# Kernel tuning notes

Hardware: AMD Instinct MI355X
Metric: run time of the kernel (lower is better)

The kernel has to match this reference:

```python
import jax, jax.numpy as jnp
import numpy as np

NUM_HEADS = 8
HEAD_DIM = 64  # joiner_dim 512 / 8
LN_EPS = 1e-5


def _layer_norm(x, g, b):
    mu = jnp.mean(x, axis=-1, keepdims=True)
    var = jnp.mean(jnp.square(x - mu), axis=-1, keepdims=True)
    return (x - mu) * jax.lax.rsqrt(var + LN_EPS) * g + b


def setup_inputs() -> dict:
    key = jax.random.key(0)
    ks = jax.random.split(key, 24)
    N, T, S = 16, 512, 5
    E, D, J, V = 512, 512, 512, 2000
    s = 0.02
    inp = {
        "encoder_out": jax.random.normal(ks[0], (N, T, S, E), jnp.float32),
        "decoder_out": jax.random.normal(ks[1], (N, T, S, D), jnp.float32),
        # ScaledLinear projections (initial_scale absorbed into weights)
        "We": jax.random.normal(ks[2], (J, E), jnp.float32) * s * 0.25,
        "be": jnp.zeros((J,), jnp.float32),
        "Wd": jax.random.normal(ks[3], (J, D), jnp.float32) * s * 0.25,
        "bd": jnp.zeros((J,), jnp.float32),
        # LayerNorms
        "g_q": jnp.ones((J,), jnp.float32),
        "beta_q": jnp.zeros((J,), jnp.float32),
        "g_kv": jnp.ones((J,), jnp.float32),
        "beta_kv": jnp.zeros((J,), jnp.float32),
        # attention projections (xavier-ish)
        "Wq": jax.random.normal(ks[4], (J, J), jnp.float32) * s,
        "bq": jnp.zeros((J,), jnp.float32),
        "Wk": jax.random.normal(ks[5], (J, J), jnp.float32) * s,
        "bk": jnp.zeros((J,), jnp.float32),
        "Wv": jax.random.normal(ks[6], (J, J), jnp.float32) * s,
        "bv": jnp.zeros((J,), jnp.float32),
        "Wo": jax.random.normal(ks[7], (J, J), jnp.float32) * s,
        "bo": jnp.zeros((J,), jnp.float32),
        # final vocab projection
        "Wout": jax.random.normal(ks[8], (V, J), jnp.float32) * s,
        "bout": jnp.zeros((V,), jnp.float32),
    }
    return inp


def reference(encoder_out, decoder_out, We, be, Wd, bd, g_q, beta_q, g_kv, beta_kv,
              Wq, bq, Wk, bk, Wv, bv, Wo, bo, Wout, bout):
    # input projections (mode == "transducer", project_input=True)
    enc = jnp.einsum('ntsc,jc->ntsj', encoder_out, We) + be
    dec = jnp.einsum('ntsc,jc->ntsj', decoder_out, Wd) + bd

    # framewise sigmoid attention
    q_in = _layer_norm(dec, g_q, beta_q)
    kv_in = _layer_norm(enc, g_kv, beta_kv)
    q = jnp.einsum('ntsj,kj->ntsk', q_in, Wq) + bq
    k = jnp.einsum('ntsj,kj->ntsk', kv_in, Wk) + bk
    v = jnp.einsum('ntsj,kj->ntsk', kv_in, Wv) + bv

    shp = q.shape[:-1]
    q = q.reshape(*shp, NUM_HEADS, HEAD_DIM)
    k = k.reshape(*shp, NUM_HEADS, HEAD_DIM)
    v = v.reshape(*shp, NUM_HEADS, HEAD_DIM)

    scale = HEAD_DIM ** -0.5
    attn = jax.nn.sigmoid(jnp.sum(q * k, axis=-1, keepdims=True) * scale)  # (N,T,S,H,1)
    context = (attn * v).reshape(*shp, NUM_HEADS * HEAD_DIM)
    context = jnp.einsum('ntsj,kj->ntsk', context, Wo) + bo

    h = jnp.tanh(dec + context)
    logits = jnp.einsum('ntsj,vj->ntsv', h, Wout) + bout
    return logits
```

## Files before the change

### kernel.cpp

```cpp
#include <hip/hip_runtime.h>
#include <stdint.h>


typedef __attribute__((ext_vector_type(8))) __bf16 bf16x8;
typedef __attribute__((ext_vector_type(4))) float float4v;
typedef __attribute__((ext_vector_type(8))) unsigned short ushort8;

static constexpr int M_TOT = 16 * 512 * 5;
static constexpr int JDIM  = 512;
static constexpr int VOUT  = 2000;
static constexpr int VPAD  = 2048;

#define DI __device__ __forceinline__

DI float bf2f(unsigned short u) {
    union { unsigned int i; float f; } w; w.i = ((unsigned int)u) << 16; return w.f;
}
DI unsigned short f2bf(float f) {
    union { float f; unsigned int i; } w; w.f = f;
    return (unsigned short)((w.i + 0x8000u) >> 16);
}

DI void gld_lds16(const void* g, void* l) {
    __builtin_amdgcn_global_load_lds(
        reinterpret_cast<__attribute__((address_space(1))) void*>(
            reinterpret_cast<uintptr_t>(g)),
        reinterpret_cast<__attribute__((address_space(3))) void*>(
            reinterpret_cast<uintptr_t>(l)),
        16, 0, 0);
}

template <int EPI, int NOUT, bool A32>
__global__ __launch_bounds__(256) void gemm_bt(
    const void* __restrict__ Ap, const unsigned short* __restrict__ B,
    const float* __restrict__ bias, void* __restrict__ Cp,
    const unsigned short* __restrict__ dres)
{
    constexpr int K = 512;
    constexpr int BM = 128, BN = 128, BK = 32;
    __shared__ unsigned short As[BM * BK];
    __shared__ unsigned short Bs[BN * BK];

    const int tid  = threadIdx.x;
    const int wave = tid >> 6;
    const int lane = tid & 63;
    const int wm   = wave >> 1;
    const int wn   = wave & 1;
    const int quad = lane >> 4;
    const int l16  = lane & 15;

    const int m0 = blockIdx.y * BM;
    const int n0 = blockIdx.x * BN;

    float4v acc[4][4];
#pragma unroll
    for (int i = 0; i < 4; i++)
#pragma unroll
        for (int j = 0; j < 4; j++)
            acc[i][j] = {0.f, 0.f, 0.f, 0.f};

    const float*          Af = (const float*)Ap;
    const unsigned short* Ab = (const unsigned short*)Ap;

    const int c0 = tid, c1 = tid + 256;
    const int ar0 = c0 >> 2, ac0 = (c0 & 3) * 8;
    const int ar1 = c1 >> 2, ac1 = (c1 & 3) * 8;

    for (int k0 = 0; k0 < K; k0 += BK) {
        gld_lds16(&B[(size_t)(n0 + ar0) * K + k0 + ac0], &Bs[c0 * 8]);
        gld_lds16(&B[(size_t)(n0 + ar1) * K + k0 + ac1], &Bs[c1 * 8]);
        if constexpr (A32) {
            const float* p0 = &Af[(size_t)(m0 + ar0) * K + k0 + ac0];
            const float* p1 = &Af[(size_t)(m0 + ar1) * K + k0 + ac1];
            float4 f0 = *(const float4*)p0;
            float4 f1 = *(const float4*)(p0 + 4);
            float4 g0 = *(const float4*)p1;
            float4 g1 = *(const float4*)(p1 + 4);
            ushort8 u0, u1;
            u0[0] = f2bf(f0.x); u0[1] = f2bf(f0.y); u0[2] = f2bf(f0.z); u0[3] = f2bf(f0.w);
            u0[4] = f2bf(f1.x); u0[5] = f2bf(f1.y); u0[6] = f2bf(f1.z); u0[7] = f2bf(f1.w);
            u1[0] = f2bf(g0.x); u1[1] = f2bf(g0.y); u1[2] = f2bf(g0.z); u1[3] = f2bf(g0.w);
            u1[4] = f2bf(g1.x); u1[5] = f2bf(g1.y); u1[6] = f2bf(g1.z); u1[7] = f2bf(g1.w);
            *reinterpret_cast<ushort8*>(&As[c0 * 8]) = u0;
            *reinterpret_cast<ushort8*>(&As[c1 * 8]) = u1;
        } else {
            gld_lds16(&Ab[(size_t)(m0 + ar0) * K + k0 + ac0], &As[c0 * 8]);
            gld_lds16(&Ab[(size_t)(m0 + ar1) * K + k0 + ac1], &As[c1 * 8]);
        }
        __syncthreads();

        bf16x8 af[4], bfv[4];
#pragma unroll
        for (int i = 0; i < 4; i++)
            af[i] = *reinterpret_cast<const bf16x8*>(
                &As[(wm * 64 + i * 16 + l16) * BK + quad * 8]);
#pragma unroll
        for (int j = 0; j < 4; j++)
            bfv[j] = *reinterpret_cast<const bf16x8*>(
                &Bs[(wn * 64 + j * 16 + l16) * BK + quad * 8]);
#pragma unroll
        for (int i = 0; i < 4; i++)
#pragma unroll
            for (int j = 0; j < 4; j++)
                acc[i][j] = __builtin_amdgcn_mfma_f32_16x16x32_bf16(
                    af[i], bfv[j], acc[i][j], 0, 0, 0);
        __syncthreads();
    }

    float bias_v[4];
#pragma unroll
    for (int j = 0; j < 4; j++) {
        int col = n0 + wn * 64 + j * 16 + l16;
        bias_v[j] = (col < NOUT) ? bias[col] : 0.f;
    }

#pragma unroll
    for (int i = 0; i < 4; i++) {
        int rbase = m0 + wm * 64 + i * 16 + quad * 4;
#pragma unroll
        for (int j = 0; j < 4; j++) {
            int col = n0 + wn * 64 + j * 16 + l16;
#pragma unroll
            for (int r = 0; r < 4; r++) {
                float val = acc[i][j][r] + bias_v[j];
                int row = rbase + r;
                if constexpr (EPI == 0) {
                    ((unsigned short*)Cp)[(size_t)row * NOUT + col] = f2bf(val);
                } else if constexpr (EPI == 2) {
                    float d = bf2f(dres[(size_t)row * 512 + col]);
                    ((unsigned short*)Cp)[(size_t)row * 512 + col] = f2bf(tanhf(d + val));
                } else {
                    if (col < NOUT)
                        ((float*)Cp)[(size_t)row * NOUT + col] = val;
                }
            }
        }
    }
}

__global__ __launch_bounds__(256) void wconv_kernel(
    const float* __restrict__ We, const float* __restrict__ Wd,
    const float* __restrict__ Wq, const float* __restrict__ Wk,
    const float* __restrict__ Wv, const float* __restrict__ Wo,
    const float* __restrict__ Wout, unsigned short* __restrict__ WB)
{
#pragma unroll
    for (int t = 0; t < 4; t++) {
        int i = blockIdx.x * 1024 + t * 256 + threadIdx.x;
        float v;
        if (i < 1572864) {
            int seg = i >> 18, off = i & 262143;
            const float* src = seg == 0 ? We : seg == 1 ? Wd : seg == 2 ? Wq
                             : seg == 3 ? Wk : seg == 4 ? Wv : Wo;
            v = src[off];
        } else {
            int rem = i - 1572864;
            int row = rem >> 9;
            v = (row < VOUT) ? Wout[rem] : 0.f;
        }
        WB[i] = f2bf(v);
    }
}

__global__ __launch_bounds__(256) void ln_kernel(
    const unsigned short* __restrict__ decO, const unsigned short* __restrict__ encO,
    const float* __restrict__ g_q, const float* __restrict__ beta_q,
    const float* __restrict__ g_kv, const float* __restrict__ beta_kv,
    unsigned short* __restrict__ q_in, unsigned short* __restrict__ kv_in)
{
    int row  = blockIdx.x * 4 + (threadIdx.x >> 6);
    int lane = threadIdx.x & 63;
    const unsigned short* src; const float *g, *bt; unsigned short* dst; int r;
    if (row < M_TOT) { src = decO; g = g_q;  bt = beta_q;  dst = q_in;  r = row; }
    else             { src = encO; g = g_kv; bt = beta_kv; dst = kv_in; r = row - M_TOT; }

    ushort8 u = *reinterpret_cast<const ushort8*>(&src[(size_t)r * 512 + lane * 8]);
    float x[8]; float s = 0.f, s2 = 0.f;
#pragma unroll
    for (int j = 0; j < 8; j++) { x[j] = bf2f(u[j]); s += x[j]; s2 += x[j] * x[j]; }
#pragma unroll
    for (int m = 1; m < 64; m <<= 1) {
        s  += __shfl_xor(s, m, 64);
        s2 += __shfl_xor(s2, m, 64);
    }
    float mean = s * (1.f / 512.f);
    float var  = s2 * (1.f / 512.f) - mean * mean;
    float rstd = rsqrtf(var + 1e-5f);
    ushort8 o;
#pragma unroll
    for (int j = 0; j < 8; j++) {
        int col = lane * 8 + j;
        o[j] = f2bf((x[j] - mean) * rstd * g[col] + bt[col]);
    }
    *reinterpret_cast<ushort8*>(&dst[(size_t)r * 512 + lane * 8]) = o;
}

__global__ __launch_bounds__(256) void attn_kernel(
    const unsigned short* __restrict__ q, const unsigned short* __restrict__ k,
    const unsigned short* __restrict__ v, unsigned short* __restrict__ ctx)
{
    int row  = blockIdx.x * 4 + (threadIdx.x >> 6);
    int lane = threadIdx.x & 63;
    size_t off = (size_t)row * 512 + lane * 8;
    ushort8 uq = *reinterpret_cast<const ushort8*>(&q[off]);
    ushort8 uk = *reinterpret_cast<const ushort8*>(&k[off]);
    float dot = 0.f;
#pragma unroll
    for (int j = 0; j < 8; j++) dot += bf2f(uq[j]) * bf2f(uk[j]);
    dot += __shfl_xor(dot, 1, 64);
    dot += __shfl_xor(dot, 2, 64);
    dot += __shfl_xor(dot, 4, 64);
    float sg = 1.f / (1.f + __expf(-dot * 0.125f));
    ushort8 uv = *reinterpret_cast<const ushort8*>(&v[off]);
    ushort8 o;
#pragma unroll
    for (int j = 0; j < 8; j++) o[j] = f2bf(sg * bf2f(uv[j]));
    *reinterpret_cast<ushort8*>(&ctx[off]) = o;
}

extern "C" void kernel_launch(void* const* d_in, const int* in_sizes, int n_in,
                              void* d_out, int out_size, void* d_ws, size_t ws_size,
                              hipStream_t stream)
{
    (void)in_sizes; (void)n_in; (void)out_size; (void)ws_size;
    const float* enc_in  = (const float*)d_in[0];
    const float* dec_in  = (const float*)d_in[1];
    const float* We      = (const float*)d_in[2];  const float* be     = (const float*)d_in[3];
    const float* Wd      = (const float*)d_in[4];  const float* bd     = (const float*)d_in[5];
    const float* g_q     = (const float*)d_in[6];  const float* beta_q = (const float*)d_in[7];
    const float* g_kv    = (const float*)d_in[8];  const float* beta_kv= (const float*)d_in[9];
    const float* Wq      = (const float*)d_in[10]; const float* bq     = (const float*)d_in[11];
    const float* Wk      = (const float*)d_in[12]; const float* bk     = (const float*)d_in[13];
    const float* Wv      = (const float*)d_in[14]; const float* bv     = (const float*)d_in[15];
    const float* Wo      = (const float*)d_in[16]; const float* bo     = (const float*)d_in[17];
    const float* Wout    = (const float*)d_in[18]; const float* bout   = (const float*)d_in[19];
    float* out = (float*)d_out;

    unsigned short* WB    = (unsigned short*)d_ws;
    unsigned short* WeB   = WB + 0;
    unsigned short* WdB   = WB + 262144;
    unsigned short* WqB   = WB + 524288;
    unsigned short* WkB   = WB + 786432;
    unsigned short* WvB   = WB + 1048576;
    unsigned short* WoB   = WB + 1310720;
    unsigned short* WoutB = WB + 1572864;

    char* sbase = (char*)d_ws + 5242880;
    const size_t SZ = (size_t)M_TOT * 512 * 2;
    unsigned short* S0 = (unsigned short*)(sbase + 0 * SZ);
    unsigned short* S1 = (unsigned short*)(sbase + 1 * SZ);
    unsigned short* S2 = (unsigned short*)(sbase + 2 * SZ);
    unsigned short* S3 = (unsigned short*)(sbase + 3 * SZ);
    unsigned short* S4 = (unsigned short*)(sbase + 4 * SZ);
    unsigned short* S5 = (unsigned short*)(sbase + 5 * SZ);

    dim3 blk(256);
    dim3 g512(JDIM / 128, M_TOT / 128);
    dim3 gout(VPAD / 128, M_TOT / 128);

    wconv_kernel<<<2560, blk, 0, stream>>>(We, Wd, Wq, Wk, Wv, Wo, Wout, WB);

    gemm_bt<0, 512, true><<<g512, blk, 0, stream>>>(enc_in, WeB, be, S0, nullptr);
    gemm_bt<0, 512, true><<<g512, blk, 0, stream>>>(dec_in, WdB, bd, S1, nullptr);

    ln_kernel<<<(2 * M_TOT) / 4, blk, 0, stream>>>(S1, S0, g_q, beta_q, g_kv, beta_kv, S2, S3);

    gemm_bt<0, 512, false><<<g512, blk, 0, stream>>>(S2, WqB, bq, S4, nullptr);
    gemm_bt<0, 512, false><<<g512, blk, 0, stream>>>(S3, WkB, bk, S0, nullptr);
    gemm_bt<0, 512, false><<<g512, blk, 0, stream>>>(S3, WvB, bv, S5, nullptr);

    attn_kernel<<<M_TOT / 4, blk, 0, stream>>>(S4, S0, S5, S2);

    gemm_bt<2, 512, false><<<g512, blk, 0, stream>>>(S2, WoB, bo, S3, S1);

    gemm_bt<3, 2000, false><<<gout, blk, 0, stream>>>(S3, WoutB, bout, out, nullptr);
}
```

Baseline: 902.9 us.

## Fold LayerNorm into projection GEMMs, merge K/V GEMM, fuse sigmoid gating into Wo GEMM

LayerNorm is removed as a separate pass. The input-projection GEMMs now accumulate per-row sum and sum-of-squares with atomics, the LN gains are pre-multiplied into Wq/Wk/Wv, and the Q/KV GEMM epilogues apply mean and rstd through precomputed column constants. K and V are computed by one GEMM with N=1024. The attention kernel now writes only per-head sigmoid scalars, which are applied to V while the Wo GEMM loads its A tile. The GEMM also moves to BK=64 with an XOR-swizzled LDS layout. In exchange it adds atomics and an extra prep kernel, and computing LN from bf16-rounded GEMM outputs algebraically changes numerics slightly.

```diff
diff --git a/kernel.cpp b/kernel.cpp
--- a/kernel.cpp
+++ b/kernel.cpp
@@ -7,9 +7,7 @@
 typedef __attribute__((ext_vector_type(8))) unsigned short ushort8;
 
 static constexpr int M_TOT = 16 * 512 * 5;
-static constexpr int JDIM  = 512;
 static constexpr int VOUT  = 2000;
-static constexpr int VPAD  = 2048;
 
 #define DI __device__ __forceinline__
 
@@ -30,16 +28,18 @@
         16, 0, 0);
 }
 
-template <int EPI, int NOUT, bool A32>
+template <int EPI, int NOUT, int ATR, int LDA>
 __global__ __launch_bounds__(256) void gemm_bt(
     const void* __restrict__ Ap, const unsigned short* __restrict__ B,
     const float* __restrict__ bias, void* __restrict__ Cp,
-    const unsigned short* __restrict__ dres)
+    const unsigned short* __restrict__ dres, const float* __restrict__ sgp,
+    const float2* __restrict__ stats, float2* __restrict__ statsOut,
+    const float* __restrict__ c1, const float* __restrict__ c2)
 {
     constexpr int K = 512;
-    constexpr int BM = 128, BN = 128, BK = 32;
+    constexpr int BM = 128, BK = 64;
     __shared__ unsigned short As[BM * BK];
-    __shared__ unsigned short Bs[BN * BK];
+    __shared__ unsigned short Bs[BM * BK];
 
     const int tid  = threadIdx.x;
     const int wave = tid >> 6;
@@ -50,7 +50,7 @@
     const int l16  = lane & 15;
 
     const int m0 = blockIdx.y * BM;
-    const int n0 = blockIdx.x * BN;
+    const int n0 = blockIdx.x * BM;
 
     float4v acc[4][4];
 #pragma unroll
@@ -62,76 +62,134 @@
     const float*          Af = (const float*)Ap;
     const unsigned short* Ab = (const unsigned short*)Ap;
 
-    const int c0 = tid, c1 = tid + 256;
-    const int ar0 = c0 >> 2, ac0 = (c0 & 3) * 8;
-    const int ar1 = c1 >> 2, ac1 = (c1 & 3) * 8;
-
     for (int k0 = 0; k0 < K; k0 += BK) {
-        gld_lds16(&B[(size_t)(n0 + ar0) * K + k0 + ac0], &Bs[c0 * 8]);
-        gld_lds16(&B[(size_t)(n0 + ar1) * K + k0 + ac1], &Bs[c1 * 8]);
-        if constexpr (A32) {
-            const float* p0 = &Af[(size_t)(m0 + ar0) * K + k0 + ac0];
-            const float* p1 = &Af[(size_t)(m0 + ar1) * K + k0 + ac1];
-            float4 f0 = *(const float4*)p0;
-            float4 f1 = *(const float4*)(p0 + 4);
-            float4 g0 = *(const float4*)p1;
-            float4 g1 = *(const float4*)(p1 + 4);
-            ushort8 u0, u1;
-            u0[0] = f2bf(f0.x); u0[1] = f2bf(f0.y); u0[2] = f2bf(f0.z); u0[3] = f2bf(f0.w);
-            u0[4] = f2bf(f1.x); u0[5] = f2bf(f1.y); u0[6] = f2bf(f1.z); u0[7] = f2bf(f1.w);
-            u1[0] = f2bf(g0.x); u1[1] = f2bf(g0.y); u1[2] = f2bf(g0.z); u1[3] = f2bf(g0.w);
-            u1[4] = f2bf(g1.x); u1[5] = f2bf(g1.y); u1[6] = f2bf(g1.z); u1[7] = f2bf(g1.w);
-            *reinterpret_cast<ushort8*>(&As[c0 * 8]) = u0;
-            *reinterpret_cast<ushort8*>(&As[c1 * 8]) = u1;
+#pragma unroll
+        for (int cc = 0; cc < 4; cc++) {
+            int s = tid + cc * 256;
+            int r = s >> 3, cs = s & 7;
+            int gc = cs ^ (r & 7);
+            gld_lds16(&B[(size_t)(n0 + r) * K + k0 + gc * 8], &Bs[s * 8]);
+        }
+        if constexpr (ATR == 0) {
+#pragma unroll
+            for (int cc = 0; cc < 4; cc++) {
+                int s = tid + cc * 256;
+                int r = s >> 3, cs = s & 7;
+                int gc = cs ^ (r & 7);
+                gld_lds16(&Ab[(size_t)(m0 + r) * LDA + k0 + gc * 8], &As[s * 8]);
+            }
+        } else if constexpr (ATR == 1) {
+#pragma unroll
+            for (int cc = 0; cc < 4; cc++) {
+                int s = tid + cc * 256;
+                int r = s >> 3, cs = s & 7;
+                int gc = cs ^ (r & 7);
+                const float* p = &Af[(size_t)(m0 + r) * LDA + k0 + gc * 8];
+                float4 f0 = *(const float4*)p;
+                float4 f1 = *(const float4*)(p + 4);
+                ushort8 u;
+                u[0] = f2bf(f0.x); u[1] = f2bf(f0.y); u[2] = f2bf(f0.z); u[3] = f2bf(f0.w);
+                u[4] = f2bf(f1.x); u[5] = f2bf(f1.y); u[6] = f2bf(f1.z); u[7] = f2bf(f1.w);
+                *reinterpret_cast<ushort8*>(&As[s * 8]) = u;
+            }
         } else {
-            gld_lds16(&Ab[(size_t)(m0 + ar0) * K + k0 + ac0], &As[c0 * 8]);
-            gld_lds16(&Ab[(size_t)(m0 + ar1) * K + k0 + ac1], &As[c1 * 8]);
+            int head = k0 >> 6;
+#pragma unroll
+            for (int cc = 0; cc < 4; cc++) {
+                int s = tid + cc * 256;
+                int r = s >> 3, cs = s & 7;
+                int gc = cs ^ (r & 7);
+                ushort8 uv = *reinterpret_cast<const ushort8*>(
+                    &Ab[(size_t)(m0 + r) * LDA + k0 + gc * 8]);
+                float sgv = sgp[(size_t)(m0 + r) * 8 + head];
+                ushort8 u;
+#pragma unroll
+                for (int t = 0; t < 8; t++) u[t] = f2bf(sgv * bf2f(uv[t]));
+                *reinterpret_cast<ushort8*>(&As[s * 8]) = u;
+            }
         }
         __syncthreads();
 
-        bf16x8 af[4], bfv[4];
-#pragma unroll
-        for (int i = 0; i < 4; i++)
-            af[i] = *reinterpret_cast<const bf16x8*>(
-                &As[(wm * 64 + i * 16 + l16) * BK + quad * 8]);
-#pragma unroll
-        for (int j = 0; j < 4; j++)
-            bfv[j] = *reinterpret_cast<const bf16x8*>(
-                &Bs[(wn * 64 + j * 16 + l16) * BK + quad * 8]);
-#pragma unroll
-        for (int i = 0; i < 4; i++)
-#pragma unroll
-            for (int j = 0; j < 4; j++)
-                acc[i][j] = __builtin_amdgcn_mfma_f32_16x16x32_bf16(
-                    af[i], bfv[j], acc[i][j], 0, 0, 0);
+#pragma unroll
+        for (int h = 0; h < 2; h++) {
+            bf16x8 af[4], bv[4];
+#pragma unroll
+            for (int i = 0; i < 4; i++) {
+                int R = wm * 64 + i * 16 + l16;
+                int c = h * 4 + quad;
+                af[i] = *reinterpret_cast<const bf16x8*>(
+                    &As[(R * 8 + (c ^ (R & 7))) * 8]);
+            }
+#pragma unroll
+            for (int j = 0; j < 4; j++) {
+                int R = wn * 64 + j * 16 + l16;
+                int c = h * 4 + quad;
+                bv[j] = *reinterpret_cast<const bf16x8*>(
+                    &Bs[(R * 8 + (c ^ (R & 7))) * 8]);
+            }
+#pragma unroll
+            for (int i = 0; i < 4; i++)
+#pragma unroll
+                for (int j = 0; j < 4; j++)
+                    acc[i][j] = __builtin_amdgcn_mfma_f32_16x16x32_bf16(
+                        af[i], bv[j], acc[i][j], 0, 0, 0);
+        }
         __syncthreads();
     }
 
-    float bias_v[4];
+    int colj[4];
+    float p0[4], p1[4];
 #pragma unroll
     for (int j = 0; j < 4; j++) {
         int col = n0 + wn * 64 + j * 16 + l16;
-        bias_v[j] = (col < NOUT) ? bias[col] : 0.f;
-    }
+        colj[j] = col;
+        if constexpr (EPI == 1) { p0[j] = c1[col]; p1[j] = c2[col]; }
+        else                    { p0[j] = (col < NOUT) ? bias[col] : 0.f; p1[j] = 0.f; }
+    }
+    unsigned short* C16 = (unsigned short*)Cp;
+    float*          Cf  = (float*)Cp;
 
 #pragma unroll
     for (int i = 0; i < 4; i++) {
         int rbase = m0 + wm * 64 + i * 16 + quad * 4;
 #pragma unroll
-        for (int j = 0; j < 4; j++) {
-            int col = n0 + wn * 64 + j * 16 + l16;
-#pragma unroll
-            for (int r = 0; r < 4; r++) {
-                float val = acc[i][j][r] + bias_v[j];
-                int row = rbase + r;
+        for (int r = 0; r < 4; r++) {
+            int row = rbase + r;
+            float mu = 0.f, rstd = 0.f, s = 0.f, ss = 0.f;
+            if constexpr (EPI == 1) {
+                float2 st = stats[row];
+                mu = st.x * (1.f / 512.f);
+                float var = st.y * (1.f / 512.f) - mu * mu;
+                rstd = rsqrtf(var + 1e-5f);
+            }
+#pragma unroll
+            for (int j = 0; j < 4; j++) {
+                float a = acc[i][j][r];
+                int col = colj[j];
                 if constexpr (EPI == 0) {
-                    ((unsigned short*)Cp)[(size_t)row * NOUT + col] = f2bf(val);
+                    float val = a + p0[j];
+                    C16[(size_t)row * NOUT + col] = f2bf(val);
+                    s += val; ss += val * val;
+                } else if constexpr (EPI == 1) {
+                    float val = rstd * a - rstd * mu * p0[j] + p1[j];
+                    C16[(size_t)row * NOUT + col] = f2bf(val);
                 } else if constexpr (EPI == 2) {
-                    float d = bf2f(dres[(size_t)row * 512 + col]);
-                    ((unsigned short*)Cp)[(size_t)row * 512 + col] = f2bf(tanhf(d + val));
+                    float val = tanhf(bf2f(dres[(size_t)row * 512 + col]) + a + p0[j]);
+                    C16[(size_t)row * 512 + col] = f2bf(val);
                 } else {
                     if (col < NOUT)
-                        ((float*)Cp)[(size_t)row * NOUT + col] = val;
+                        Cf[(size_t)row * NOUT + col] = a + p0[j];
+                }
+            }
+            if constexpr (EPI == 0) {
+                s  += __shfl_xor(s, 1, 64);  s  += __shfl_xor(s, 2, 64);
+                s  += __shfl_xor(s, 4, 64);  s  += __shfl_xor(s, 8, 64);
+                ss += __shfl_xor(ss, 1, 64); ss += __shfl_xor(ss, 2, 64);
+                ss += __shfl_xor(ss, 4, 64); ss += __shfl_xor(ss, 8, 64);
+                if (l16 == 0) {
+                    float* sp = (float*)&statsOut[row];
+                    atomicAdd(sp + 0, s);
+                    atomicAdd(sp + 1, ss);
                 }
             }
         }
@@ -142,7 +200,9 @@
     const float* __restrict__ We, const float* __restrict__ Wd,
     const float* __restrict__ Wq, const float* __restrict__ Wk,
     const float* __restrict__ Wv, const float* __restrict__ Wo,
-    const float* __restrict__ Wout, unsigned short* __restrict__ WB)
+    const float* __restrict__ Wout,
+    const float* __restrict__ g_q, const float* __restrict__ g_kv,
+    unsigned short* __restrict__ WB)
 {
 #pragma unroll
     for (int t = 0; t < 4; t++) {
@@ -153,6 +213,8 @@
             const float* src = seg == 0 ? We : seg == 1 ? Wd : seg == 2 ? Wq
                              : seg == 3 ? Wk : seg == 4 ? Wv : Wo;
             v = src[off];
+            if (seg == 2) v *= g_q[off & 511];
+            else if (seg == 3 || seg == 4) v *= g_kv[off & 511];
         } else {
             int rem = i - 1572864;
             int row = rem >> 9;
@@ -162,60 +224,64 @@
     }
 }
 
-__global__ __launch_bounds__(256) void ln_kernel(
-    const unsigned short* __restrict__ decO, const unsigned short* __restrict__ encO,
+__global__ __launch_bounds__(256) void prep_kernel(
+    const float* __restrict__ Wq, const float* __restrict__ Wk,
+    const float* __restrict__ Wv,
     const float* __restrict__ g_q, const float* __restrict__ beta_q,
     const float* __restrict__ g_kv, const float* __restrict__ beta_kv,
-    unsigned short* __restrict__ q_in, unsigned short* __restrict__ kv_in)
+    const float* __restrict__ bq, const float* __restrict__ bk,
+    const float* __restrict__ bv,
+    float* __restrict__ c1q, float* __restrict__ c2q,
+    float* __restrict__ c1kv, float* __restrict__ c2kv,
+    float* __restrict__ stats_zero)
+{
+    int b = blockIdx.x;
+    if (b < 384) {
+        int row  = b * 4 + (threadIdx.x >> 6);
+        int lane = threadIdx.x & 63;
+        const float* W  = row < 512 ? Wq : (row < 1024 ? Wk : Wv);
+        int wrow        = row < 512 ? row : (row < 1024 ? row - 512 : row - 1024);
+        const float* g  = row < 512 ? g_q : g_kv;
+        const float* bt = row < 512 ? beta_q : beta_kv;
+        float bias      = row < 512 ? bq[row] : (row < 1024 ? bk[row - 512] : bv[row - 1024]);
+        float* o1 = row < 512 ? &c1q[row] : &c1kv[row - 512];
+        float* o2 = row < 512 ? &c2q[row] : &c2kv[row - 512];
+        float s1 = 0.f, s2 = 0.f;
+#pragma unroll
+        for (int t = 0; t < 8; t++) {
+            int j = lane * 8 + t;
+            float w = W[(size_t)wrow * 512 + j];
+            s1 += w * g[j]; s2 += w * bt[j];
+        }
+#pragma unroll
+        for (int m = 1; m < 64; m <<= 1) {
+            s1 += __shfl_xor(s1, m, 64);
+            s2 += __shfl_xor(s2, m, 64);
+        }
+        if (lane == 0) { *o1 = s1; *o2 = s2 + bias; }
+    } else {
+        int base = (b - 384) * 1024 + threadIdx.x;
+#pragma unroll
+        for (int t = 0; t < 4; t++) stats_zero[base + t * 256] = 0.f;
+    }
+}
+
+__global__ __launch_bounds__(256) void sg_kernel(
+    const unsigned short* __restrict__ q, const unsigned short* __restrict__ kv,
+    float* __restrict__ sgbuf)
 {
     int row  = blockIdx.x * 4 + (threadIdx.x >> 6);
     int lane = threadIdx.x & 63;
-    const unsigned short* src; const float *g, *bt; unsigned short* dst; int r;
-    if (row < M_TOT) { src = decO; g = g_q;  bt = beta_q;  dst = q_in;  r = row; }
-    else             { src = encO; g = g_kv; bt = beta_kv; dst = kv_in; r = row - M_TOT; }
-
-    ushort8 u = *reinterpret_cast<const ushort8*>(&src[(size_t)r * 512 + lane * 8]);
-    float x[8]; float s = 0.f, s2 = 0.f;
-#pragma unroll
-    for (int j = 0; j < 8; j++) { x[j] = bf2f(u[j]); s += x[j]; s2 += x[j] * x[j]; }
-#pragma unroll
-    for (int m = 1; m < 64; m <<= 1) {
-        s  += __shfl_xor(s, m, 64);
-        s2 += __shfl_xor(s2, m, 64);
-    }
-    float mean = s * (1.f / 512.f);
-    float var  = s2 * (1.f / 512.f) - mean * mean;
-    float rstd = rsqrtf(var + 1e-5f);
-    ushort8 o;
-#pragma unroll
-    for (int j = 0; j < 8; j++) {
-        int col = lane * 8 + j;
-        o[j] = f2bf((x[j] - mean) * rstd * g[col] + bt[col]);
-    }
-    *reinterpret_cast<ushort8*>(&dst[(size_t)r * 512 + lane * 8]) = o;
-}
-
-__global__ __launch_bounds__(256) void attn_kernel(
-    const unsigned short* __restrict__ q, const unsigned short* __restrict__ k,
-    const unsigned short* __restrict__ v, unsigned short* __restrict__ ctx)
-{
-    int row  = blockIdx.x * 4 + (threadIdx.x >> 6);
-    int lane = threadIdx.x & 63;
-    size_t off = (size_t)row * 512 + lane * 8;
-    ushort8 uq = *reinterpret_cast<const ushort8*>(&q[off]);
-    ushort8 uk = *reinterpret_cast<const ushort8*>(&k[off]);
+    ushort8 uq = *reinterpret_cast<const ushort8*>(&q[(size_t)row * 512 + lane * 8]);
+    ushort8 uk = *reinterpret_cast<const ushort8*>(&kv[(size_t)row * 1024 + lane * 8]);
     float dot = 0.f;
 #pragma unroll
     for (int j = 0; j < 8; j++) dot += bf2f(uq[j]) * bf2f(uk[j]);
     dot += __shfl_xor(dot, 1, 64);
     dot += __shfl_xor(dot, 2, 64);
     dot += __shfl_xor(dot, 4, 64);
-    float sg = 1.f / (1.f + __expf(-dot * 0.125f));
-    ushort8 uv = *reinterpret_cast<const ushort8*>(&v[off]);
-    ushort8 o;
-#pragma unroll
-    for (int j = 0; j < 8; j++) o[j] = f2bf(sg * bf2f(uv[j]));
-    *reinterpret_cast<ushort8*>(&ctx[off]) = o;
+    if ((lane & 7) == 0)
+        sgbuf[(size_t)row * 8 + (lane >> 3)] = 1.f / (1.f + __expf(-dot * 0.125f));
 }
 
 extern "C" void kernel_launch(void* const* d_in, const int* in_sizes, int n_in,
@@ -240,38 +306,52 @@
     unsigned short* WeB   = WB + 0;
     unsigned short* WdB   = WB + 262144;
     unsigned short* WqB   = WB + 524288;
-    unsigned short* WkB   = WB + 786432;
-    unsigned short* WvB   = WB + 1048576;
+    unsigned short* WkvB  = WB + 786432;
     unsigned short* WoB   = WB + 1310720;
     unsigned short* WoutB = WB + 1572864;
 
-    char* sbase = (char*)d_ws + 5242880;
+    float* FB = (float*)((char*)d_ws + 5242880);
+    float* c1q  = FB;
+    float* c2q  = FB + 512;
+    float* c1kv = FB + 1024;
+    float* c2kv = FB + 2048;
+    float2* stats_dec = (float2*)(FB + 3072);
+    float2* stats_enc = stats_dec + M_TOT;
+    float*  sgbuf     = FB + 3072 + 4 * M_TOT;
+    float*  stats_zero = FB + 3072;
+
+    char* sbase = (char*)d_ws + 7221248;
     const size_t SZ = (size_t)M_TOT * 512 * 2;
     unsigned short* S0 = (unsigned short*)(sbase + 0 * SZ);
     unsigned short* S1 = (unsigned short*)(sbase + 1 * SZ);
     unsigned short* S2 = (unsigned short*)(sbase + 2 * SZ);
-    unsigned short* S3 = (unsigned short*)(sbase + 3 * SZ);
-    unsigned short* S4 = (unsigned short*)(sbase + 4 * SZ);
-    unsigned short* S5 = (unsigned short*)(sbase + 5 * SZ);
+    unsigned short* S3 = (unsigned short*)(sbase + 4 * SZ);
+    unsigned short* S4 = (unsigned short*)(sbase + 5 * SZ);
 
     dim3 blk(256);
-    dim3 g512(JDIM / 128, M_TOT / 128);
-    dim3 gout(VPAD / 128, M_TOT / 128);
-
-    wconv_kernel<<<2560, blk, 0, stream>>>(We, Wd, Wq, Wk, Wv, Wo, Wout, WB);
-
-    gemm_bt<0, 512, true><<<g512, blk, 0, stream>>>(enc_in, WeB, be, S0, nullptr);
-    gemm_bt<0, 512, true><<<g512, blk, 0, stream>>>(dec_in, WdB, bd, S1, nullptr);
-
-    ln_kernel<<<(2 * M_TOT) / 4, blk, 0, stream>>>(S1, S0, g_q, beta_q, g_kv, beta_kv, S2, S3);
-
-    gemm_bt<0, 512, false><<<g512, blk, 0, stream>>>(S2, WqB, bq, S4, nullptr);
-    gemm_bt<0, 512, false><<<g512, blk, 0, stream>>>(S3, WkB, bk, S0, nullptr);
-    gemm_bt<0, 512, false><<<g512, blk, 0, stream>>>(S3, WvB, bv, S5, nullptr);
-
-    attn_kernel<<<M_TOT / 4, blk, 0, stream>>>(S4, S0, S5, S2);
-
-    gemm_bt<2, 512, false><<<g512, blk, 0, stream>>>(S2, WoB, bo, S3, S1);
-
-    gemm_bt<3, 2000, false><<<gout, blk, 0, stream>>>(S3, WoutB, bout, out, nullptr);
-}
+    dim3 g512(4, 320);
+    dim3 g1024(8, 320);
+    dim3 gout(16, 320);
+
+    wconv_kernel<<<2560, blk, 0, stream>>>(We, Wd, Wq, Wk, Wv, Wo, Wout, g_q, g_kv, WB);
+    prep_kernel<<<544, blk, 0, stream>>>(Wq, Wk, Wv, g_q, beta_q, g_kv, beta_kv,
+                                         bq, bk, bv, c1q, c2q, c1kv, c2kv, stats_zero);
+
+    gemm_bt<0, 512, 1, 512><<<g512, blk, 0, stream>>>(
+        enc_in, WeB, be, S0, nullptr, nullptr, nullptr, stats_enc, nullptr, nullptr);
+    gemm_bt<0, 512, 1, 512><<<g512, blk, 0, stream>>>(
+        dec_in, WdB, bd, S1, nullptr, nullptr, nullptr, stats_dec, nullptr, nullptr);
+
+    gemm_bt<1, 512, 0, 512><<<g512, blk, 0, stream>>>(
+        S1, WqB, nullptr, S4, nullptr, nullptr, stats_dec, nullptr, c1q, c2q);
+    gemm_bt<1, 1024, 0, 512><<<g1024, blk, 0, stream>>>(
+        S0, WkvB, nullptr, S2, nullptr, nullptr, stats_enc, nullptr, c1kv, c2kv);
+
+    sg_kernel<<<M_TOT / 4, blk, 0, stream>>>(S4, S2, sgbuf);
+
+    gemm_bt<2, 512, 2, 1024><<<g512, blk, 0, stream>>>(
+        S2 + 512, WoB, bo, S3, S1, sgbuf, nullptr, nullptr, nullptr, nullptr);
+
+    gemm_bt<3, 2000, 0, 512><<<gout, blk, 0, stream>>>(
+        S3, WoutB, bout, out, nullptr, nullptr, nullptr, nullptr, nullptr, nullptr);
+}
```

New measurement: 975.7 us. 1.08x slower.
